# Kernel optimization log

Hardware: AMD Instinct MI355X
Metric: run time of the kernel (lower is better)

The kernel has to match this reference:

```python
import jax, jax.numpy as jnp
import numpy as np

B, S, D = 2, 2048, 4096
NH, NKV, HD = 32, 8, 128
GROUPS = NH // NKV
SCALE = HD ** -0.5


def _rotate_half(x):
    x1, x2 = x[..., : HD // 2], x[..., HD // 2 :]
    return jnp.concatenate((-x2, x1), axis=-1)


def setup_inputs() -> dict:
    key = jax.random.key(0)
    ks = jax.random.split(key, 6)
    hidden_states = jax.random.normal(ks[0], (B, S, D), dtype=jnp.float32)
    # Real RoPE tables: cos/sin of shape [B, S, HD]
    inv_freq = 1.0 / (10000.0 ** (jnp.arange(0, HD, 2, dtype=jnp.float32) / HD))
    pos = jnp.arange(S, dtype=jnp.float32)
    freqs = pos[:, None] * inv_freq[None, :]            # [S, HD/2]
    emb = jnp.concatenate((freqs, freqs), axis=-1)       # [S, HD]
    cos = jnp.broadcast_to(jnp.cos(emb)[None], (B, S, HD))
    sin = jnp.broadcast_to(jnp.sin(emb)[None], (B, S, HD))
    std = D ** -0.5
    wq = jax.random.normal(ks[1], (NH * HD, D), dtype=jnp.float32) * std
    wk = jax.random.normal(ks[2], (NKV * HD, D), dtype=jnp.float32) * std
    wv = jax.random.normal(ks[3], (NKV * HD, D), dtype=jnp.float32) * std
    wo = jax.random.normal(ks[4], (D, NH * HD), dtype=jnp.float32) * std
    return {"hidden_states": hidden_states, "cos": cos, "sin": sin,
            "wq": wq, "wk": wk, "wv": wv, "wo": wo}


def reference(hidden_states, cos, sin, wq, wk, wv, wo):
    bsz, q_len, _ = hidden_states.shape
    # projections (nn.Linear: y = x @ W.T), reshape to [B, H, S, HD]
    q = (hidden_states @ wq.T).reshape(bsz, q_len, NH, HD).transpose(0, 2, 1, 3)
    k = (hidden_states @ wk.T).reshape(bsz, q_len, NKV, HD).transpose(0, 2, 1, 3)
    v = (hidden_states @ wv.T).reshape(bsz, q_len, NKV, HD).transpose(0, 2, 1, 3)
    # RoPE, cos/sin broadcast over head dim
    c, s = cos[:, None], sin[:, None]
    q = q * c + _rotate_half(q) * s
    k = k * c + _rotate_half(k) * s
    # GQA repeat_kv: [B, NKV, S, HD] -> [B, NH, S, HD]
    k = jnp.repeat(k, GROUPS, axis=1)
    v = jnp.repeat(v, GROUPS, axis=1)
    scores = jnp.einsum("bhqd,bhkd->bhqk", q, k) * SCALE
    causal = jnp.triu(jnp.ones((q_len, q_len), dtype=bool), k=1)
    scores = jnp.where(causal[None, None], -jnp.inf, scores)
    attn = jax.nn.softmax(scores.astype(jnp.float32), axis=-1).astype(q.dtype)
    out = jnp.einsum("bhqk,bhkd->bhqd", attn, v)
    out = out.transpose(0, 2, 1, 3).reshape(bsz, q_len, NH * HD)
    return out @ wo.T
```

## Files before the change

kernel.cpp:

```cpp
#include <hip/hip_runtime.h>

#define B_    2
#define S_    2048
#define D_    4096
#define NH_   32
#define NKV_  8
#define HD_   128
#define M_TOK 4096
#define NQKV  6144
#define SCALE 0.08838834764831845f

typedef unsigned short u16;
typedef unsigned int   u32;
typedef __attribute__((ext_vector_type(8))) short short8;
typedef __attribute__((ext_vector_type(4))) float floatx4;
typedef __attribute__((ext_vector_type(16))) float floatx16;

typedef const __attribute__((address_space(1))) void cg_void;
typedef __attribute__((address_space(3))) void lds_void;
#define GP(x) ((cg_void*)(x))
#define LP(x) ((lds_void*)(x))

__device__ inline u16 f2bf(float f) {
    u32 u = __float_as_uint(f);
    u = (u + 0x7FFFu + ((u >> 16) & 1u)) >> 16;
    return (u16)u;
}
__device__ inline float bf2f(u16 u) {
    return __uint_as_float(((u32)u) << 16);
}
__device__ inline u32 cvt_pk_bf16(float a, float b) {
    u32 r;
    asm("v_cvt_pk_bf16_f32 %0, %1, %2" : "=v"(r) : "v"(a), "v"(b));
    return r;
}

__global__ __launch_bounds__(256) void cvt_bf16(
    const float* __restrict__ src, u16* __restrict__ dst, int n8)
{
    int id = blockIdx.x * 256 + threadIdx.x;
    if (id >= n8) return;
    size_t i = (size_t)id * 8;
    float4 a = *(const float4*)(src + i);
    float4 b = *(const float4*)(src + i + 4);
    __align__(16) u16 t[8];
    t[0] = f2bf(a.x); t[1] = f2bf(a.y); t[2] = f2bf(a.z); t[3] = f2bf(a.w);
    t[4] = f2bf(b.x); t[5] = f2bf(b.y); t[6] = f2bf(b.z); t[7] = f2bf(b.w);
    *(short8*)(dst + i) = *(short8*)t;
}

#define GBK 64
#define A_U16 (256 * GBK)
#define B_U16 (128 * GBK)
#define BUF_U16 (A_U16 + B_U16)

template<bool OUT_F32>
__global__ __launch_bounds__(512) void gemm_pipe(
    const u16* __restrict__ A, const u16* __restrict__ Bw,
    void* __restrict__ Cp, int M, int N, int K)
{
    __shared__ __align__(16) u16 smem[2][BUF_U16];

    const int tid  = threadIdx.x;
    const int lane = tid & 63, wave = tid >> 6;
    const int quad = lane >> 4, l16 = lane & 15;

    const int gx  = gridDim.x;
    const int lin = blockIdx.y * gx + blockIdx.x;
    const int nwg = gx * gridDim.y;
    const int wg  = (lin & 7) * (nwg >> 3) + (lin >> 3);
    const int by  = wg / gx, bx = wg - by * gx;
    const int m0 = by * 256, n0 = bx * 128;

    const int wm = (wave >> 1) * 64;
    const int wn = (wave & 1) * 64;

    const int srow  = tid >> 3;
    const int sslot = tid & 7;
    const u16* Asrc = A  + (size_t)(m0 + srow) * K + (size_t)((sslot ^ (srow & 7)) * 8);
    const u16* Bsrc = Bw + (size_t)(n0 + srow) * K + (size_t)((sslot ^ (srow & 7)) * 8);

    const int NT = K / GBK;
    const int sw = l16 & 7;

    floatx4 acc[4][4];
    #pragma unroll
    for (int i = 0; i < 4; ++i)
        #pragma unroll
        for (int j = 0; j < 4; ++j) acc[i][j] = (floatx4){0.f, 0.f, 0.f, 0.f};

    #pragma unroll
    for (int tb = 0; tb < 2; ++tb) {
        u16* Ad = &smem[tb][0]     + tid * 8;
        u16* Bd = &smem[tb][A_U16] + tid * 8;
        const size_t k0 = (size_t)tb * GBK;
        #pragma unroll
        for (int q = 0; q < 4; ++q)
            __builtin_amdgcn_global_load_lds(GP(Asrc + (size_t)q * 64 * K + k0),
                                             LP(Ad + q * 4096), 16, 0, 0);
        #pragma unroll
        for (int q = 0; q < 2; ++q)
            __builtin_amdgcn_global_load_lds(GP(Bsrc + (size_t)q * 64 * K + k0),
                                             LP(Bd + q * 4096), 16, 0, 0);
    }
    __builtin_amdgcn_sched_barrier(0);
    asm volatile("s_waitcnt vmcnt(6)" ::: "memory");
    __builtin_amdgcn_sched_barrier(0);
    __builtin_amdgcn_s_barrier();

    #pragma unroll 1
    for (int t = 0; t < NT; ++t) {
        const u16* Ab = &smem[t & 1][0]     + (size_t)(wm + l16) * GBK;
        const u16* Bb = &smem[t & 1][A_U16] + (size_t)(wn + l16) * GBK;

        #pragma unroll
        for (int kh = 0; kh < 2; ++kh) {
            const int sl = ((kh * 4 + quad) ^ sw) * 8;
            short8 af[4], bfv[4];
            #pragma unroll
            for (int i = 0; i < 4; ++i)
                af[i] = *(const short8*)(Ab + i * 16 * GBK + sl);
            #pragma unroll
            for (int j = 0; j < 4; ++j)
                bfv[j] = *(const short8*)(Bb + j * 16 * GBK + sl);

            __builtin_amdgcn_s_barrier();
            __builtin_amdgcn_s_setprio(1);
            #pragma unroll
            for (int i = 0; i < 4; ++i)
                #pragma unroll
                for (int j = 0; j < 4; ++j)
                    acc[i][j] = __builtin_amdgcn_mfma_f32_16x16x32_bf16(
                        af[i], bfv[j], acc[i][j], 0, 0, 0);
            __builtin_amdgcn_s_setprio(0);
            __builtin_amdgcn_s_barrier();
        }

        if (t + 1 == NT) break;

        __builtin_amdgcn_sched_barrier(0);
        if (t + 2 < NT) {
            u16* Ad = &smem[t & 1][0]     + tid * 8;
            u16* Bd = &smem[t & 1][A_U16] + tid * 8;
            const size_t k0 = (size_t)(t + 2) * GBK;
            #pragma unroll
            for (int q = 0; q < 4; ++q)
                __builtin_amdgcn_global_load_lds(GP(Asrc + (size_t)q * 64 * K + k0),
                                                 LP(Ad + q * 4096), 16, 0, 0);
            #pragma unroll
            for (int q = 0; q < 2; ++q)
                __builtin_amdgcn_global_load_lds(GP(Bsrc + (size_t)q * 64 * K + k0),
                                                 LP(Bd + q * 4096), 16, 0, 0);
            __builtin_amdgcn_sched_barrier(0);
            asm volatile("s_waitcnt vmcnt(6)" ::: "memory");
        } else {
            asm volatile("s_waitcnt vmcnt(0)" ::: "memory");
        }
        __builtin_amdgcn_sched_barrier(0);
        __builtin_amdgcn_s_barrier();
    }

    #pragma unroll
    for (int i = 0; i < 4; ++i)
        #pragma unroll
        for (int j = 0; j < 4; ++j)
            #pragma unroll
            for (int r = 0; r < 4; ++r) {
                int row = m0 + wm + i * 16 + quad * 4 + r;
                int col = n0 + wn + j * 16 + l16;
                float v = acc[i][j][r];
                if constexpr (OUT_F32)
                    ((float*)Cp)[(size_t)row * N + col] = v;
                else
                    ((u16*)Cp)[(size_t)row * N + col] = f2bf(v);
            }
}

__global__ __launch_bounds__(256) void rope_reshape(
    const u16* __restrict__ qkv, const float* __restrict__ cosp,
    const float* __restrict__ sinp, u16* __restrict__ Q, u16* __restrict__ Kb)
{
    const size_t QN = (size_t)M_TOK * NH_ * 64;
    size_t id = (size_t)blockIdx.x * 256 + threadIdx.x;
    if (id < QN) {
        int j = id & 63; int h = (id >> 6) & (NH_ - 1); int tok = (int)(id >> 11);
        int b = tok >> 11, s = tok & (S_ - 1);
        float c  = cosp[(size_t)tok * HD_ + j];
        float sn = sinp[(size_t)tok * HD_ + j];
        float x1 = bf2f(qkv[(size_t)tok * NQKV + h * HD_ + j]);
        float x2 = bf2f(qkv[(size_t)tok * NQKV + h * HD_ + 64 + j]);
        size_t o = ((size_t)(b * NH_ + h) * S_ + s) * HD_ + j;
        Q[o]      = f2bf(x1 * c - x2 * sn);
        Q[o + 64] = f2bf(x2 * c + x1 * sn);
    } else {
        size_t kid = id - QN;
        int j = kid & 63; int h = (kid >> 6) & (NKV_ - 1); int tok = (int)(kid >> 9);
        int b = tok >> 11, s = tok & (S_ - 1);
        float c  = cosp[(size_t)tok * HD_ + j];
        float sn = sinp[(size_t)tok * HD_ + j];
        float x1 = bf2f(qkv[(size_t)tok * NQKV + 4096 + h * HD_ + j]);
        float x2 = bf2f(qkv[(size_t)tok * NQKV + 4096 + h * HD_ + 64 + j]);
        size_t o = ((size_t)(b * NKV_ + h) * S_ + s) * HD_ + j;
        Kb[o]      = f2bf(x1 * c - x2 * sn);
        Kb[o + 64] = f2bf(x2 * c + x1 * sn);
    }
}

__global__ __launch_bounds__(256) void v_transpose(
    const u16* __restrict__ qkv, u16* __restrict__ Vt)
{
    __shared__ __align__(16) u16 T[128][136];
    int bidx = blockIdx.x;
    int st = bidx & 15; int h = (bidx >> 4) & 7; int b = bidx >> 7;
    int s0 = st * 128;
    int tid = threadIdx.x;
    #pragma unroll
    for (int i = 0; i < 8; ++i) {
        int row = i * 16 + (tid >> 4); int cg = tid & 15;
        const u16* src = qkv + (size_t)(b * S_ + s0 + row) * NQKV + 5120 + h * HD_ + cg * 8;
        *(short8*)&T[row][cg * 8] = *(const short8*)src;
    }
    __syncthreads();
    #pragma unroll
    for (int i = 0; i < 8; ++i) {
        int d = i * 16 + (tid >> 4); int cg = tid & 15;
        __align__(16) u16 tmp[8];
        #pragma unroll
        for (int j = 0; j < 8; ++j) tmp[j] = T[cg * 8 + j][d];
        *(short8*)(Vt + ((size_t)(b * NKV_ + h) * HD_ + d) * S_ + s0 + cg * 8) =
            *(short8*)tmp;
    }
}

__global__ __launch_bounds__(256) void flash_attn(
    const u16* __restrict__ Q, const u16* __restrict__ Kb,
    const u16* __restrict__ Vt, u16* __restrict__ AO)
{
    __shared__ __align__(16) u16 smem[2][8192];

    const int tid  = threadIdx.x;
    const int wave = tid >> 6, lane = tid & 63;
    const int l31 = lane & 31, hi = lane >> 5;

    const int i    = blockIdx.x;
    const int xcd  = i & 7;
    const int slot = i >> 3;
    const int g    = slot & 3;
    const int qb   = 15 - ((slot >> 2) & 15);
    const int b    = slot >> 6;
    const int hk   = xcd;
    const int h    = hk * 4 + g;
    const int qt   = qb * 4 + wave;
    const int q0   = qt * 32;
    const int qpos = q0 + l31;
    const int TB   = qb * 4 + 4;

    const u16* Kbase = Kb + (size_t)(b * NKV_ + hk) * S_ * HD_;
    const u16* Vbase = Vt + (size_t)(b * NKV_ + hk) * HD_ * S_;

    const u16* Qp = Q + ((size_t)(b * NH_ + h) * S_ + q0 + l31) * HD_ + hi * 8;
    short8 qf[8];
    #pragma unroll
    for (int c = 0; c < 8; ++c) qf[c] = *(const short8*)(Qp + c * 16);
    __builtin_amdgcn_sched_barrier(0);
    asm volatile("s_waitcnt vmcnt(0)" ::: "memory");
    __builtin_amdgcn_sched_barrier(0);

    const int gk0 = tid, gk1 = tid + 256;
    const int kdsl0 = gk0 >> 5, kkv0 = gk0 & 31;
    const int kdsl1 = gk1 >> 5, kkv1 = gk1 & 31;
    const int vks0 = gk0 >> 7, vd0 = gk0 & 127;
    const int vks1 = gk1 >> 7, vd1 = gk1 & 127;

    #define STAGE_KV(kb_, buf_)                                                        \
        do {                                                                           \
            u16* Ksd = &smem[buf_][0];                                                 \
            u16* Vsd = &smem[buf_][4096];                                              \
            __builtin_amdgcn_global_load_lds(                                          \
                GP(Kbase + (size_t)((kb_) + kkv0) * HD_ + kdsl0 * 8),                  \
                LP(Ksd + gk0 * 8), 16, 0, 0);                                          \
            __builtin_amdgcn_global_load_lds(                                          \
                GP(Kbase + (size_t)((kb_) + kkv1) * HD_ + kdsl1 * 8),                  \
                LP(Ksd + gk1 * 8), 16, 0, 0);                                          \
            __builtin_amdgcn_global_load_lds(                                          \
                GP(Vbase + (size_t)vd0 * S_ + (kb_) + vks0 * 8),                       \
                LP(Vsd + gk0 * 8), 16, 0, 0);                                          \
            __builtin_amdgcn_global_load_lds(                                          \
                GP(Vbase + (size_t)vd1 * S_ + (kb_) + vks1 * 8),                       \
                LP(Vsd + gk1 * 8), 16, 0, 0);                                          \
        } while (0)

    float m = -1e30f, l = 0.f;
    floatx16 o[4];
    #pragma unroll
    for (int n = 0; n < 4; ++n)
        #pragma unroll
        for (int r = 0; r < 16; ++r) o[n][r] = 0.f;

    STAGE_KV(0, 0);
    STAGE_KV(32, 1);
    __builtin_amdgcn_sched_barrier(0);
    asm volatile("s_waitcnt vmcnt(4)" ::: "memory");
    __builtin_amdgcn_sched_barrier(0);
    __builtin_amdgcn_s_barrier();

    #pragma unroll 1
    for (int t = 0; t < TB; ++t) {
        const u16* Ks = &smem[t & 1][0];
        const u16* Vs = &smem[t & 1][4096];

        if (t <= qt) {
            const int kb = t * 32;

            floatx16 ca, cb;
            #pragma unroll
            for (int r = 0; r < 16; ++r) { ca[r] = 0.f; cb[r] = 0.f; }
            __builtin_amdgcn_s_setprio(1);
            #pragma unroll
            for (int c = 0; c < 8; c += 2) {
                ca = __builtin_amdgcn_mfma_f32_32x32x16_bf16(
                    *(const short8*)(Ks + (2 * c + hi) * 256 + l31 * 8),
                    qf[c], ca, 0, 0, 0);
                cb = __builtin_amdgcn_mfma_f32_32x32x16_bf16(
                    *(const short8*)(Ks + (2 * (c + 1) + hi) * 256 + l31 * 8),
                    qf[c + 1], cb, 0, 0, 0);
            }
            __builtin_amdgcn_s_setprio(0);

            float s[16];
            #pragma unroll
            for (int r = 0; r < 16; ++r) s[r] = ca[r] + cb[r];

            if (t == qt) {
                #pragma unroll
                for (int r = 0; r < 16; ++r) {
                    const int kvr = (r & 3) + 8 * (r >> 2) + 4 * hi;
                    if (kb + kvr > qpos) s[r] = -1e38f;
                }
            }

            float b0 = fmaxf(fmaxf(s[0], s[1]), fmaxf(s[2], s[3]));
            float b1 = fmaxf(fmaxf(s[4], s[5]), fmaxf(s[6], s[7]));
            float b2 = fmaxf(fmaxf(s[8], s[9]), fmaxf(s[10], s[11]));
            float b3 = fmaxf(fmaxf(s[12], s[13]), fmaxf(s[14], s[15]));
            float bm = fmaxf(fmaxf(b0, b1), fmaxf(b2, b3));
            bm = fmaxf(bm, __shfl_xor(bm, 32));
            const float bmS = bm * SCALE;

            if (__any(bmS > m)) {
                const float mn = fmaxf(m, bmS);
                const float al = __expf(m - mn);
                m = mn;
                l *= al;
                #pragma unroll
                for (int n = 0; n < 4; ++n)
                    #pragma unroll
                    for (int r = 0; r < 16; ++r) o[n][r] *= al;
            }

            float p[16];
            float rs = 0.f;
            #pragma unroll
            for (int r = 0; r < 16; ++r) {
                p[r] = __expf(fmaf(s[r], SCALE, -m));
                rs += p[r];
            }
            rs += __shfl_xor(rs, 32);
            l += rs;

            u32 P01 = cvt_pk_bf16(p[0],  p[1]);
            u32 P23 = cvt_pk_bf16(p[2],  p[3]);
            u32 P45 = cvt_pk_bf16(p[4],  p[5]);
            u32 P67 = cvt_pk_bf16(p[6],  p[7]);
            u32 P89 = cvt_pk_bf16(p[8],  p[9]);
            u32 Pab = cvt_pk_bf16(p[10], p[11]);
            u32 Pcd = cvt_pk_bf16(p[12], p[13]);
            u32 Pef = cvt_pk_bf16(p[14], p[15]);
            u32 x1 = __shfl_xor(hi ? P01 : P45, 32);
            u32 x2 = __shfl_xor(hi ? P23 : P67, 32);
            u32 x3 = __shfl_xor(hi ? P89 : Pcd, 32);
            u32 x4 = __shfl_xor(hi ? Pab : Pef, 32);

            union { short8 v; u32 w[4]; } f0, f1;
            f0.w[0] = hi ? x1 : P01;  f0.w[1] = hi ? x2 : P23;
            f0.w[2] = hi ? P45 : x1;  f0.w[3] = hi ? P67 : x2;
            f1.w[0] = hi ? x3 : P89;  f1.w[1] = hi ? x4 : Pab;
            f1.w[2] = hi ? Pcd : x3;  f1.w[3] = hi ? Pef : x4;

            __builtin_amdgcn_s_setprio(1);
            #pragma unroll
            for (int n = 0; n < 4; ++n) {
                o[n] = __builtin_amdgcn_mfma_f32_32x32x16_bf16(
                    *(const short8*)(Vs + (hi) * 1024 + (n * 32 + l31) * 8),
                    f0.v, o[n], 0, 0, 0);
                o[n] = __builtin_amdgcn_mfma_f32_32x32x16_bf16(
                    *(const short8*)(Vs + (2 + hi) * 1024 + (n * 32 + l31) * 8),
                    f1.v, o[n], 0, 0, 0);
            }
            __builtin_amdgcn_s_setprio(0);
        }

        __builtin_amdgcn_s_barrier();
        __builtin_amdgcn_sched_barrier(0);
        if (t + 2 < TB) {
            STAGE_KV((t + 2) * 32, t & 1);
            __builtin_amdgcn_sched_barrier(0);
            asm volatile("s_waitcnt vmcnt(4)" ::: "memory");
        } else if (t + 1 < TB) {
            asm volatile("s_waitcnt vmcnt(0)" ::: "memory");
        }
        __builtin_amdgcn_sched_barrier(0);
        __builtin_amdgcn_s_barrier();
    }
    #undef STAGE_KV

    const float inv = 1.0f / l;
    u16* dst = AO + ((size_t)(b * S_) + q0 + l31) * (NH_ * HD_) + h * HD_ + hi * 4;
    #pragma unroll
    for (int n = 0; n < 4; ++n)
        #pragma unroll
        for (int rg = 0; rg < 4; ++rg) {
            u32 lo  = cvt_pk_bf16(o[n][rg * 4 + 0] * inv, o[n][rg * 4 + 1] * inv);
            u32 hi2 = cvt_pk_bf16(o[n][rg * 4 + 2] * inv, o[n][rg * 4 + 3] * inv);
            *(uint2*)(dst + n * 32 + rg * 8) = make_uint2(lo, hi2);
        }
}

extern "C" void kernel_launch(void* const* d_in, const int* in_sizes, int n_in,
                              void* d_out, int out_size, void* d_ws, size_t ws_size,
                              hipStream_t stream)
{
    const float* hs   = (const float*)d_in[0];
    const float* cosp = (const float*)d_in[1];
    const float* sinp = (const float*)d_in[2];
    const float* wq   = (const float*)d_in[3];
    const float* wk   = (const float*)d_in[4];
    const float* wv   = (const float*)d_in[5];
    const float* wo   = (const float*)d_in[6];
    float* out = (float*)d_out;
    char* ws = (char*)d_ws;

    const size_t MB = 1024 * 1024;
    u16* qkv_raw = (u16*)ws;
    u16* AO      = (u16*)ws;
    u16* Wqkv    = (u16*)(ws + 48 * MB);
    u16* Qb      = (u16*)(ws + 48 * MB);
    u16* Kb      = (u16*)(ws + 80 * MB);
    u16* Vt      = (u16*)(ws + 88 * MB);
    u16* hs_bf   = (u16*)(ws + 96 * MB);
    u16* Wo_bf   = (u16*)(ws + 96 * MB);

    cvt_bf16<<<8192, 256, 0, stream>>>(hs, hs_bf, (M_TOK * D_) / 8);
    cvt_bf16<<<8192, 256, 0, stream>>>(wq, Wqkv, (NH_ * HD_ * D_) / 8);
    cvt_bf16<<<2048, 256, 0, stream>>>(wk, Wqkv + (size_t)NH_ * HD_ * D_, (NKV_ * HD_ * D_) / 8);
    cvt_bf16<<<2048, 256, 0, stream>>>(wv, Wqkv + (size_t)(NH_ + NKV_) * HD_ * D_, (NKV_ * HD_ * D_) / 8);

    gemm_pipe<false><<<dim3(NQKV / 128, M_TOK / 256), 512, 0, stream>>>(
        hs_bf, Wqkv, qkv_raw, M_TOK, NQKV, D_);

    rope_reshape<<<40960, 256, 0, stream>>>(qkv_raw, cosp, sinp, Qb, Kb);

    v_transpose<<<256, 256, 0, stream>>>(qkv_raw, Vt);

    flash_attn<<<1024, 256, 0, stream>>>(Qb, Kb, Vt, AO);

    cvt_bf16<<<8192, 256, 0, stream>>>(wo, Wo_bf, (D_ * NH_ * HD_) / 8);

    gemm_pipe<true><<<dim3(D_ / 128, M_TOK / 256), 512, 0, stream>>>(
        AO, Wo_bf, out, M_TOK, D_, NH_ * HD_);
}
```

Baseline: 785.9 us.

## Enlarge GEMM block tile to 256x256 with 2x4 wave layout

The pipelined bf16 GEMM now uses a 256x256 output tile per workgroup instead of 256x128. Each of the 8 waves computes a 128x64 sub-tile with 32 accumulators, and LDS per stage grows to hold B at 256 rows. The per-k-half barriers and setprio around the MFMA block are removed, leaving one barrier per k-tile. The aim is more reuse of each LDS fragment per MFMA and less synchronisation, at the cost of more registers and LDS, which may lower occupancy, and half as many workgroups on the grid.

```diff
diff --git a/kernel.cpp b/kernel.cpp
--- a/kernel.cpp
+++ b/kernel.cpp
@@ -50,16 +50,16 @@
 }
 
 #define GBK 64
-#define A_U16 (256 * GBK)
-#define B_U16 (128 * GBK)
-#define BUF_U16 (A_U16 + B_U16)
+#define TA_U16 (256 * GBK)
+#define TB_U16 (256 * GBK)
+#define TBUF_U16 (TA_U16 + TB_U16)
 
 template<bool OUT_F32>
 __global__ __launch_bounds__(512) void gemm_pipe(
     const u16* __restrict__ A, const u16* __restrict__ Bw,
     void* __restrict__ Cp, int M, int N, int K)
 {
-    __shared__ __align__(16) u16 smem[2][BUF_U16];
+    __shared__ __align__(16) u16 smem[2][TBUF_U16];
 
     const int tid  = threadIdx.x;
     const int lane = tid & 63, wave = tid >> 6;
@@ -70,105 +70,96 @@
     const int nwg = gx * gridDim.y;
     const int wg  = (lin & 7) * (nwg >> 3) + (lin >> 3);
     const int by  = wg / gx, bx = wg - by * gx;
-    const int m0 = by * 256, n0 = bx * 128;
-
-    const int wm = (wave >> 1) * 64;
-    const int wn = (wave & 1) * 64;
-
-    const int srow  = tid >> 3;
-    const int sslot = tid & 7;
-    const u16* Asrc = A  + (size_t)(m0 + srow) * K + (size_t)((sslot ^ (srow & 7)) * 8);
-    const u16* Bsrc = Bw + (size_t)(n0 + srow) * K + (size_t)((sslot ^ (srow & 7)) * 8);
+    const int m0 = by * 256, n0 = bx * 256;
+
+    const int wr = wave >> 2;
+    const int wc = wave & 3;
 
     const int NT = K / GBK;
     const int sw = l16 & 7;
 
-    floatx4 acc[4][4];
-    #pragma unroll
-    for (int i = 0; i < 4; ++i)
+    #define STAGE(t_, buf_)                                                          \
+        do {                                                                         \
+            const size_t kk_ = (size_t)(t_) * GBK;                                   \
+            _Pragma("unroll")                                                        \
+            for (int q = 0; q < 4; ++q) {                                            \
+                const int g_ = q * 512 + tid;                                        \
+                const int r_ = g_ >> 3, s_ = g_ & 7;                                 \
+                __builtin_amdgcn_global_load_lds(                                    \
+                    GP(A + (size_t)(m0 + r_) * K + kk_ + ((s_ ^ (r_ & 7)) * 8)),     \
+                    LP(&smem[buf_][0] + (size_t)g_ * 8), 16, 0, 0);                  \
+            }                                                                        \
+            _Pragma("unroll")                                                        \
+            for (int q = 0; q < 4; ++q) {                                            \
+                const int g_ = q * 512 + tid;                                        \
+                const int r_ = g_ >> 3, s_ = g_ & 7;                                 \
+                __builtin_amdgcn_global_load_lds(                                    \
+                    GP(Bw + (size_t)(n0 + r_) * K + kk_ + ((s_ ^ (r_ & 7)) * 8)),    \
+                    LP(&smem[buf_][TA_U16] + (size_t)g_ * 8), 16, 0, 0);             \
+            }                                                                        \
+        } while (0)
+
+    floatx4 acc[8][4];
+    #pragma unroll
+    for (int i = 0; i < 8; ++i)
         #pragma unroll
         for (int j = 0; j < 4; ++j) acc[i][j] = (floatx4){0.f, 0.f, 0.f, 0.f};
 
-    #pragma unroll
-    for (int tb = 0; tb < 2; ++tb) {
-        u16* Ad = &smem[tb][0]     + tid * 8;
-        u16* Bd = &smem[tb][A_U16] + tid * 8;
-        const size_t k0 = (size_t)tb * GBK;
-        #pragma unroll
-        for (int q = 0; q < 4; ++q)
-            __builtin_amdgcn_global_load_lds(GP(Asrc + (size_t)q * 64 * K + k0),
-                                             LP(Ad + q * 4096), 16, 0, 0);
-        #pragma unroll
-        for (int q = 0; q < 2; ++q)
-            __builtin_amdgcn_global_load_lds(GP(Bsrc + (size_t)q * 64 * K + k0),
-                                             LP(Bd + q * 4096), 16, 0, 0);
-    }
-    __builtin_amdgcn_sched_barrier(0);
-    asm volatile("s_waitcnt vmcnt(6)" ::: "memory");
+    const int abase = (wr * 128 + l16) * 64;
+    const int bbase = TA_U16 + (wc * 64 + l16) * 64;
+
+    STAGE(0, 0);
+    STAGE(1, 1);
+    __builtin_amdgcn_sched_barrier(0);
+    asm volatile("s_waitcnt vmcnt(8)" ::: "memory");
     __builtin_amdgcn_sched_barrier(0);
     __builtin_amdgcn_s_barrier();
 
     #pragma unroll 1
     for (int t = 0; t < NT; ++t) {
-        const u16* Ab = &smem[t & 1][0]     + (size_t)(wm + l16) * GBK;
-        const u16* Bb = &smem[t & 1][A_U16] + (size_t)(wn + l16) * GBK;
+        const u16* Sb = &smem[t & 1][0];
 
         #pragma unroll
         for (int kh = 0; kh < 2; ++kh) {
-            const int sl = ((kh * 4 + quad) ^ sw) * 8;
-            short8 af[4], bfv[4];
-            #pragma unroll
-            for (int i = 0; i < 4; ++i)
-                af[i] = *(const short8*)(Ab + i * 16 * GBK + sl);
-            #pragma unroll
-            for (int j = 0; j < 4; ++j)
-                bfv[j] = *(const short8*)(Bb + j * 16 * GBK + sl);
-
-            __builtin_amdgcn_s_barrier();
-            __builtin_amdgcn_s_setprio(1);
-            #pragma unroll
-            for (int i = 0; i < 4; ++i)
+            const int p = ((kh * 4 + quad) ^ sw) * 8;
+            short8 af[8], bfv[4];
+            #pragma unroll
+            for (int m = 0; m < 8; ++m)
+                af[m] = *(const short8*)(Sb + abase + m * 1024 + p);
+            #pragma unroll
+            for (int n = 0; n < 4; ++n)
+                bfv[n] = *(const short8*)(Sb + bbase + n * 1024 + p);
+            #pragma unroll
+            for (int m = 0; m < 8; ++m)
                 #pragma unroll
-                for (int j = 0; j < 4; ++j)
-                    acc[i][j] = __builtin_amdgcn_mfma_f32_16x16x32_bf16(
-                        af[i], bfv[j], acc[i][j], 0, 0, 0);
-            __builtin_amdgcn_s_setprio(0);
-            __builtin_amdgcn_s_barrier();
+                for (int n = 0; n < 4; ++n)
+                    acc[m][n] = __builtin_amdgcn_mfma_f32_16x16x32_bf16(
+                        af[m], bfv[n], acc[m][n], 0, 0, 0);
         }
 
-        if (t + 1 == NT) break;
-
+        __builtin_amdgcn_s_barrier();
         __builtin_amdgcn_sched_barrier(0);
         if (t + 2 < NT) {
-            u16* Ad = &smem[t & 1][0]     + tid * 8;
-            u16* Bd = &smem[t & 1][A_U16] + tid * 8;
-            const size_t k0 = (size_t)(t + 2) * GBK;
-            #pragma unroll
-            for (int q = 0; q < 4; ++q)
-                __builtin_amdgcn_global_load_lds(GP(Asrc + (size_t)q * 64 * K + k0),
-                                                 LP(Ad + q * 4096), 16, 0, 0);
-            #pragma unroll
-            for (int q = 0; q < 2; ++q)
-                __builtin_amdgcn_global_load_lds(GP(Bsrc + (size_t)q * 64 * K + k0),
-                                                 LP(Bd + q * 4096), 16, 0, 0);
+            STAGE(t + 2, t & 1);
             __builtin_amdgcn_sched_barrier(0);
-            asm volatile("s_waitcnt vmcnt(6)" ::: "memory");
-        } else {
+            asm volatile("s_waitcnt vmcnt(8)" ::: "memory");
+        } else if (t + 1 < NT) {
             asm volatile("s_waitcnt vmcnt(0)" ::: "memory");
         }
         __builtin_amdgcn_sched_barrier(0);
         __builtin_amdgcn_s_barrier();
     }
-
-    #pragma unroll
-    for (int i = 0; i < 4; ++i)
-        #pragma unroll
-        for (int j = 0; j < 4; ++j)
+    #undef STAGE
+
+    #pragma unroll
+    for (int m = 0; m < 8; ++m)
+        #pragma unroll
+        for (int n = 0; n < 4; ++n)
             #pragma unroll
             for (int r = 0; r < 4; ++r) {
-                int row = m0 + wm + i * 16 + quad * 4 + r;
-                int col = n0 + wn + j * 16 + l16;
-                float v = acc[i][j][r];
+                int row = m0 + wr * 128 + m * 16 + quad * 4 + r;
+                int col = n0 + wc * 64 + n * 16 + l16;
+                float v = acc[m][n][r];
                 if constexpr (OUT_F32)
                     ((float*)Cp)[(size_t)row * N + col] = v;
                 else
@@ -455,7 +446,7 @@
     cvt_bf16<<<2048, 256, 0, stream>>>(wk, Wqkv + (size_t)NH_ * HD_ * D_, (NKV_ * HD_ * D_) / 8);
     cvt_bf16<<<2048, 256, 0, stream>>>(wv, Wqkv + (size_t)(NH_ + NKV_) * HD_ * D_, (NKV_ * HD_ * D_) / 8);
 
-    gemm_pipe<false><<<dim3(NQKV / 128, M_TOK / 256), 512, 0, stream>>>(
+    gemm_pipe<false><<<dim3(NQKV / 256, M_TOK / 256), 512, 0, stream>>>(
         hs_bf, Wqkv, qkv_raw, M_TOK, NQKV, D_);
 
     rope_reshape<<<40960, 256, 0, stream>>>(qkv_raw, cosp, sinp, Qb, Kb);
@@ -466,6 +457,6 @@
 
     cvt_bf16<<<8192, 256, 0, stream>>>(wo, Wo_bf, (D_ * NH_ * HD_) / 8);
 
-    gemm_pipe<true><<<dim3(D_ / 128, M_TOK / 256), 512, 0, stream>>>(
+    gemm_pipe<true><<<dim3(D_ / 256, M_TOK / 256), 512, 0, stream>>>(
         AO, Wo_bf, out, M_TOK, D_, NH_ * HD_);
 }
```

After: 732.4 us. 6.8% less time.
